# Performance work log

Measured on AMD Instinct MI355X. Metric: run time of the kernel, lower is better.

Reference implementation:

```python
import jax, jax.numpy as jnp
import numpy as np

N_API, N_FILE, E = 50000, 20000, 250000
N_INP, N_OUT, H = 512, 256, 3


def setup_inputs() -> dict:
    key = jax.random.key(0)
    ks = jax.random.split(key, 16)
    s = 0.05
    return {
        "emb_api": jax.random.normal(ks[0], (N_API, N_INP), jnp.float32),
        "emb_file": jax.random.normal(ks[1], (N_FILE, N_INP), jnp.float32),
        "e_tensor": jax.random.normal(ks[2], (E,), jnp.float32),
        "src": jax.random.randint(ks[3], (E,), 0, N_API, jnp.int32),
        "dst": jax.random.randint(ks[4], (E,), 0, N_FILE, jnp.int32),
        # api_proj / file_proj (Linear n_inp->n_inp), stored as [in,out]
        "Wapi": jax.random.normal(ks[5], (N_INP, N_INP), jnp.float32) * s,
        "bapi": jnp.zeros((N_INP,), jnp.float32),
        "Wfile": jax.random.normal(ks[6], (N_INP, N_INP), jnp.float32) * s,
        "bfile": jnp.zeros((N_INP,), jnp.float32),
        # GATConv fc_src / fc_dst (no bias), attn vectors, output bias
        "Wsrc": jax.random.normal(ks[7], (N_INP, H * N_OUT), jnp.float32) * s,
        "Wdst": jax.random.normal(ks[8], (N_INP, H * N_OUT), jnp.float32) * s,
        "attn_l": jax.random.normal(ks[9], (H, N_OUT), jnp.float32) * s,
        "attn_r": jax.random.normal(ks[10], (H, N_OUT), jnp.float32) * s,
        "gat_bias": jnp.zeros((H * N_OUT,), jnp.float32),
        # head_linear (3*n_out -> n_out)
        "Whead": jax.random.normal(ks[11], (H * N_OUT, N_OUT), jnp.float32) * s,
        "bhead": jnp.zeros((N_OUT,), jnp.float32),
    }


def reference(emb_api, emb_file, e_tensor, src, dst,
              Wapi, bapi, Wfile, bfile,
              Wsrc, Wdst, attn_l, attn_r, gat_bias,
              Whead, bhead):
    nd = emb_file.shape[0]
    # dual linear projections
    x_api = emb_api @ Wapi + bapi            # [Nsrc, n_inp]
    x_file = emb_file @ Wfile + bfile        # [Ndst, n_inp]
    # GATConv (bipartite, DGL semantics): per-head linear, additive attention
    fsrc = (x_api @ Wsrc).reshape(-1, H, N_OUT)   # [Nsrc, H, D]
    fdst = (x_file @ Wdst).reshape(-1, H, N_OUT)  # [Ndst, H, D]
    el = jnp.sum(fsrc * attn_l, axis=-1)          # [Nsrc, H]
    er = jnp.sum(fdst * attn_r, axis=-1)          # [Ndst, H]
    e = jax.nn.leaky_relu(el[src] + er[dst], 0.2)  # [E, H]
    # edge softmax over incoming edges of each dst node
    m = jax.ops.segment_max(e, dst, num_segments=nd)   # [Ndst, H]
    a = jnp.exp(e - m[dst])
    z = jax.ops.segment_sum(a, dst, num_segments=nd)   # [Ndst, H]
    alpha = a / z[dst]                                  # [E, H]
    # weighted aggregation of source messages
    rst = jax.ops.segment_sum(alpha[:, :, None] * fsrc[src], dst,
                              num_segments=nd)          # [Ndst, H, D]
    rst = rst + gat_bias.reshape(H, N_OUT)
    # head fusion
    z_str = rst.reshape(nd, H * N_OUT) @ Whead + bhead  # [Ndst, n_out]
    return z_str
```

## Files before the change

### kernel.cpp

```cpp
#include <hip/hip_runtime.h>
#include <hip/hip_bf16.h>
#include <cstdint>
#include <cstddef>

#define N_INP 512
#define N_OUT 256
#define H 3
#define HD (H * N_OUT)
#define AGG_D (H * (N_INP + 1))
#define HSTR 522
#define KP 1568
#define GEMM_NT (KP / 32)

typedef __attribute__((ext_vector_type(8))) short short8;
typedef __attribute__((ext_vector_type(4))) float f32x4;

__device__ inline unsigned short f2bf(float x) {
    union { float f; unsigned u; } v; v.f = x;
    unsigned r = v.u + 0x7fffu + ((v.u >> 16) & 1u);
    return (unsigned short)(r >> 16);
}
__device__ inline float bflo2f(unsigned u) {
    union { unsigned u; float f; } v; v.u = u << 16; return v.f;
}
__device__ inline float bfhi2f(unsigned u) {
    union { unsigned u; float f; } v; v.u = u & 0xffff0000u; return v.f;
}

__global__ void zero_int_kernel(int* p, int n) {
    int i = blockIdx.x * blockDim.x + threadIdx.x;
    if (i < n) p[i] = 0;
}

__global__ __launch_bounds__(256) void v_kernel(
    const float* __restrict__ Wsrc, const float* __restrict__ Wdst,
    const float* __restrict__ attn_l, const float* __restrict__ attn_r,
    float* __restrict__ v) {
    int wave = threadIdx.x >> 6, lane = threadIdx.x & 63;
    int idx = blockIdx.x * 4 + wave;
    if (idx >= 2 * H * N_INP) return;
    int which = idx / (H * N_INP);
    int r = idx % (H * N_INP);
    int h = r / N_INP, o = r % N_INP;
    const float* W = which ? Wdst : Wsrc;
    const float* at = which ? attn_r : attn_l;
    float s = 0.f;
#pragma unroll
    for (int i = 0; i < N_OUT / 64; ++i) {
        int t = lane + i * 64;
        s += W[(size_t)o * HD + h * N_OUT + t] * at[h * N_OUT + t];
    }
#pragma unroll
    for (int off = 32; off >= 1; off >>= 1) s += __shfl_xor(s, off, 64);
    if (lane == 0) v[idx] = s;
}

__global__ __launch_bounds__(256) void u_kernel(
    const float* __restrict__ Wapi, const float* __restrict__ Wfile,
    const float* __restrict__ bapi, const float* __restrict__ bfile,
    const float* __restrict__ v, float* __restrict__ u,
    float* __restrict__ ebias) {
    int wave = threadIdx.x >> 6, lane = threadIdx.x & 63;
    int idx = blockIdx.x * 4 + wave;
    if (idx < 2 * H * N_INP) {
        int which = idx / (H * N_INP);
        int r = idx % (H * N_INP);
        int h = r / N_INP, i = r % N_INP;
        const float* W = which ? Wfile : Wapi;
        const float* vv = v + which * (H * N_INP) + h * N_INP;
        float s = 0.f;
#pragma unroll
        for (int j = 0; j < N_INP / 64; ++j) {
            int o = lane + j * 64;
            s += W[(size_t)i * N_INP + o] * vv[o];
        }
#pragma unroll
        for (int off = 32; off >= 1; off >>= 1) s += __shfl_xor(s, off, 64);
        if (lane == 0) u[idx] = s;
    } else if (idx < 2 * H * N_INP + 6) {
        int k = idx - 2 * H * N_INP;
        int which = k / H, h = k % H;
        const float* b = which ? bfile : bapi;
        const float* vv = v + which * (H * N_INP) + h * N_INP;
        float s = 0.f;
#pragma unroll
        for (int j = 0; j < N_INP / 64; ++j) {
            int o = lane + j * 64;
            s += b[o] * vv[o];
        }
#pragma unroll
        for (int off = 32; off >= 1; off >>= 1) s += __shfl_xor(s, off, 64);
        if (lane == 0) ebias[k] = s;
    }
}

__global__ __launch_bounds__(256) void elr_kernel(
    const float* __restrict__ emb, const float* __restrict__ u,
    const float* __restrict__ ebias, float* __restrict__ out,
    unsigned short* __restrict__ embB, int n) {
    __shared__ float su[H * N_INP];
    for (int i = threadIdx.x; i < H * N_INP; i += 256) su[i] = u[i];
    __syncthreads();
    int wave = threadIdx.x >> 6;
    int lane = threadIdx.x & 63;
    int node = blockIdx.x * 4 + wave;
    if (node >= n) return;
    const float4* row = (const float4*)(emb + (size_t)node * N_INP);
    float4 v0 = row[lane];
    float4 v1 = row[64 + lane];
    int c0 = lane * 4, c1 = 256 + lane * 4;
    if (embB) {
        unsigned short* o = embB + (size_t)node * N_INP;
        ushort4 p0, p1;
        p0.x = f2bf(v0.x); p0.y = f2bf(v0.y); p0.z = f2bf(v0.z); p0.w = f2bf(v0.w);
        p1.x = f2bf(v1.x); p1.y = f2bf(v1.y); p1.z = f2bf(v1.z); p1.w = f2bf(v1.w);
        *(ushort4*)(o + c0) = p0;
        *(ushort4*)(o + c1) = p1;
    }
    float d[H];
#pragma unroll
    for (int h = 0; h < H; ++h) {
        const float* uh = su + h * N_INP;
        d[h] = v0.x * uh[c0] + v0.y * uh[c0 + 1] + v0.z * uh[c0 + 2] + v0.w * uh[c0 + 3]
             + v1.x * uh[c1] + v1.y * uh[c1 + 1] + v1.z * uh[c1 + 2] + v1.w * uh[c1 + 3];
#pragma unroll
        for (int off = 32; off >= 1; off >>= 1) d[h] += __shfl_xor(d[h], off, 64);
    }
    if (lane == 0) {
#pragma unroll
        for (int h = 0; h < H; ++h) out[(size_t)node * H + h] = d[h] + ebias[h];
    }
}

__global__ void count_kernel(const int* __restrict__ dst, int* __restrict__ counts, int E) {
    int e = blockIdx.x * blockDim.x + threadIdx.x;
    if (e < E) atomicAdd(&counts[dst[e]], 1);
}

__global__ __launch_bounds__(1024) void scan_kernel(const int* __restrict__ counts,
                                                    int* __restrict__ offsets,
                                                    int* __restrict__ cursor, int n) {
    __shared__ int part[1024];
    int t = threadIdx.x;
    const int CH = (n + 1023) / 1024;
    int lo = t * CH, hi = min(lo + CH, n);
    int s = 0;
    for (int i = lo; i < hi; ++i) s += counts[i];
    part[t] = s;
    __syncthreads();
    for (int off = 1; off < 1024; off <<= 1) {
        int v = (t >= off) ? part[t - off] : 0;
        __syncthreads();
        part[t] += v;
        __syncthreads();
    }
    int base = (t == 0) ? 0 : part[t - 1];
    for (int i = lo; i < hi; ++i) {
        offsets[i] = base; cursor[i] = base;
        base += counts[i];
    }
    if (t == 1023) offsets[n] = part[1023];
}

__global__ void scatter_kernel(const int* __restrict__ src, const int* __restrict__ dst,
                               int* __restrict__ cursor, int* __restrict__ csr_src, int E) {
    int e = blockIdx.x * blockDim.x + threadIdx.x;
    if (e < E) {
        int slot = atomicAdd(&cursor[dst[e]], 1);
        csr_src[slot] = src[e];
    }
}

__global__ __launch_bounds__(256) void alpha_kernel(
    const int* __restrict__ offsets, const int* __restrict__ csr_src,
    const float* __restrict__ el, const float* __restrict__ er,
    float* __restrict__ alpha, int nd) {
    int wave = threadIdx.x >> 6;
    int lane = threadIdx.x & 63;
    int d = blockIdx.x * 4 + wave;
    if (d >= nd) return;
    int lo = offsets[d], hi = offsets[d + 1];
    if (lo == hi) return;
    float er0 = er[(size_t)d * H + 0], er1 = er[(size_t)d * H + 1], er2 = er[(size_t)d * H + 2];
    float m0 = -3.4e38f, m1 = -3.4e38f, m2 = -3.4e38f;
    for (int s = lo + lane; s < hi; s += 64) {
        int u = csr_src[s];
        float e0 = el[(size_t)u * H + 0] + er0; e0 = e0 >= 0.f ? e0 : 0.2f * e0;
        float e1 = el[(size_t)u * H + 1] + er1; e1 = e1 >= 0.f ? e1 : 0.2f * e1;
        float e2 = el[(size_t)u * H + 2] + er2; e2 = e2 >= 0.f ? e2 : 0.2f * e2;
        m0 = fmaxf(m0, e0); m1 = fmaxf(m1, e1); m2 = fmaxf(m2, e2);
    }
#pragma unroll
    for (int off = 32; off >= 1; off >>= 1) {
        m0 = fmaxf(m0, __shfl_xor(m0, off, 64));
        m1 = fmaxf(m1, __shfl_xor(m1, off, 64));
        m2 = fmaxf(m2, __shfl_xor(m2, off, 64));
    }
    float s0 = 0.f, s1 = 0.f, s2 = 0.f;
    for (int s = lo + lane; s < hi; s += 64) {
        int u = csr_src[s];
        float e0 = el[(size_t)u * H + 0] + er0; e0 = e0 >= 0.f ? e0 : 0.2f * e0;
        float e1 = el[(size_t)u * H + 1] + er1; e1 = e1 >= 0.f ? e1 : 0.2f * e1;
        float e2 = el[(size_t)u * H + 2] + er2; e2 = e2 >= 0.f ? e2 : 0.2f * e2;
        float a0 = expf(e0 - m0), a1 = expf(e1 - m1), a2 = expf(e2 - m2);
        alpha[(size_t)s * H + 0] = a0; alpha[(size_t)s * H + 1] = a1; alpha[(size_t)s * H + 2] = a2;
        s0 += a0; s1 += a1; s2 += a2;
    }
#pragma unroll
    for (int off = 32; off >= 1; off >>= 1) {
        s0 += __shfl_xor(s0, off, 64);
        s1 += __shfl_xor(s1, off, 64);
        s2 += __shfl_xor(s2, off, 64);
    }
    float i0 = 1.f / s0, i1 = 1.f / s1, i2 = 1.f / s2;
    for (int s = lo + lane; s < hi; s += 64) {
        alpha[(size_t)s * H + 0] *= i0;
        alpha[(size_t)s * H + 1] *= i1;
        alpha[(size_t)s * H + 2] *= i2;
    }
}

#define AGG_CH 512
__global__ __launch_bounds__(256) void agg_kernel(
    const int* __restrict__ offsets, const int* __restrict__ csr_src,
    const float* __restrict__ alpha, const unsigned short* __restrict__ embB,
    unsigned short* __restrict__ aggB, int nd) {
    __shared__ int su[AGG_CH];
    __shared__ float sw0[AGG_CH], sw1[AGG_CH], sw2[AGG_CH];
    int d = blockIdx.x;
    if (d >= nd) return;
    int tid = threadIdx.x;
    int lo = offsets[d], hi = offsets[d + 1];
    const unsigned* ebdw = (const unsigned*)embB;
    float a00 = 0.f, a01 = 0.f, a10 = 0.f, a11 = 0.f, a20 = 0.f, a21 = 0.f;
    for (int base = lo; base < hi; base += AGG_CH) {
        int cnt = min(hi - base, AGG_CH);
        for (int i = tid; i < cnt; i += 256) {
            int s = base + i;
            su[i] = csr_src[s];
            sw0[i] = alpha[(size_t)s * H + 0];
            sw1[i] = alpha[(size_t)s * H + 1];
            sw2[i] = alpha[(size_t)s * H + 2];
        }
        __syncthreads();
        int i = 0;
        for (; i + 4 <= cnt; i += 4) {
            int u0 = su[i], u1 = su[i + 1], u2 = su[i + 2], u3 = su[i + 3];
            unsigned v0 = ebdw[((size_t)u0 << 8) + tid];
            unsigned v1 = ebdw[((size_t)u1 << 8) + tid];
            unsigned v2 = ebdw[((size_t)u2 << 8) + tid];
            unsigned v3 = ebdw[((size_t)u3 << 8) + tid];
            float w00 = sw0[i], w01 = sw1[i], w02 = sw2[i];
            float w10 = sw0[i+1], w11 = sw1[i+1], w12 = sw2[i+1];
            float w20 = sw0[i+2], w21 = sw1[i+2], w22 = sw2[i+2];
            float w30 = sw0[i+3], w31 = sw1[i+3], w32 = sw2[i+3];
            float x, y;
            x = bflo2f(v0); y = bfhi2f(v0);
            a00 += w00 * x; a01 += w00 * y; a10 += w01 * x; a11 += w01 * y; a20 += w02 * x; a21 += w02 * y;
            x = bflo2f(v1); y = bfhi2f(v1);
            a00 += w10 * x; a01 += w10 * y; a10 += w11 * x; a11 += w11 * y; a20 += w12 * x; a21 += w12 * y;
            x = bflo2f(v2); y = bfhi2f(v2);
            a00 += w20 * x; a01 += w20 * y; a10 += w21 * x; a11 += w21 * y; a20 += w22 * x; a21 += w22 * y;
            x = bflo2f(v3); y = bfhi2f(v3);
            a00 += w30 * x; a01 += w30 * y; a10 += w31 * x; a11 += w31 * y; a20 += w32 * x; a21 += w32 * y;
        }
        for (; i < cnt; ++i) {
            int u = su[i];
            unsigned v = ebdw[((size_t)u << 8) + tid];
            float w0 = sw0[i], w1 = sw1[i], w2 = sw2[i];
            float x = bflo2f(v), y = bfhi2f(v);
            a00 += w0 * x; a01 += w0 * y;
            a10 += w1 * x; a11 += w1 * y;
            a20 += w2 * x; a21 += w2 * y;
        }
        __syncthreads();
    }
    int c = tid * 2;
    size_t base = (size_t)d * KP;
    *(unsigned*)(aggB + base + 0 * HSTR + c) = (unsigned)f2bf(a00) | ((unsigned)f2bf(a01) << 16);
    *(unsigned*)(aggB + base + 1 * HSTR + c) = (unsigned)f2bf(a10) | ((unsigned)f2bf(a11) << 16);
    *(unsigned*)(aggB + base + 2 * HSTR + c) = (unsigned)f2bf(a20) | ((unsigned)f2bf(a21) << 16);
    if (tid == 0) {
        unsigned short flag = (hi > lo) ? (unsigned short)0x3f80 : (unsigned short)0;
#pragma unroll
        for (int h = 0; h < H; ++h) {
            aggB[base + h * HSTR + 512] = flag;
            for (int z = 513; z < HSTR; ++z) aggB[base + h * HSTR + z] = 0;
        }
        aggB[base + 3 * HSTR + 0] = 0;
        aggB[base + 3 * HSTR + 1] = 0;
    }
}

template <int K>
__global__ __launch_bounds__(256) void wgemm(
    const float* __restrict__ A, int lda, size_t sAz,
    const float* __restrict__ B, int ldb, size_t sBz,
    float* __restrict__ C, int ldc, size_t sCz, int M) {
    A += blockIdx.z * sAz; B += blockIdx.z * sBz; C += blockIdx.z * sCz;
    __shared__ float sA[8 * K];
    __shared__ float red[8 * 256];
    int tid = threadIdx.x;
    int r0 = blockIdx.x * 8;
    int bn = blockIdx.y * 64;
    for (int i = tid; i < 8 * K; i += 256) {
        int r = i / K, k = i % K;
        sA[i] = A[(size_t)(r0 + r) * lda + k];
    }
    __syncthreads();
    int cl = tid & 63, ks = tid >> 6;
    int col = bn + cl;
    const int KC = K / 4;
    float acc[8] = {};
    for (int k0 = ks * KC; k0 < ks * KC + KC; k0 += 8) {
        float b[8];
#pragma unroll
        for (int j = 0; j < 8; ++j) b[j] = B[(size_t)(k0 + j) * ldb + col];
#pragma unroll
        for (int j = 0; j < 8; ++j) {
            float bb = b[j];
#pragma unroll
            for (int i = 0; i < 8; ++i) acc[i] += sA[i * K + k0 + j] * bb;
        }
    }
#pragma unroll
    for (int i = 0; i < 8; ++i) red[i * 256 + ks * 64 + cl] = acc[i];
    __syncthreads();
    for (int t = tid; t < 512; t += 256) {
        int i = t >> 6, c = t & 63;
        float s = red[i * 256 + c] + red[i * 256 + 64 + c]
                + red[i * 256 + 128 + c] + red[i * 256 + 192 + c];
        if (r0 + i < M) C[(size_t)(r0 + i) * ldc + bn + c] = s;
    }
}

__global__ __launch_bounds__(256) void brow_kernel(
    const float* __restrict__ bapi, const float* __restrict__ T,
    const float* __restrict__ gat_bias, const float* __restrict__ Whead,
    const float* __restrict__ bhead,
    float* __restrict__ Mmat, float* __restrict__ bz) {
    int wave = threadIdx.x >> 6, lane = threadIdx.x & 63;
    int idx = blockIdx.x * 4 + wave;
    if (idx < H * N_OUT) {
        int h = idx / N_OUT, j = idx % N_OUT;
        float s = 0.f;
#pragma unroll
        for (int i = 0; i < N_INP / 64; ++i) {
            int cc = lane + i * 64;
            s += bapi[cc] * T[((size_t)h * N_INP + cc) * N_OUT + j];
        }
#pragma unroll
        for (int off = 32; off >= 1; off >>= 1) s += __shfl_xor(s, off, 64);
        if (lane == 0) Mmat[((size_t)(h * 513 + 512)) * N_OUT + j] = s;
    } else if (idx < H * N_OUT + N_OUT) {
        int j = idx - H * N_OUT;
        float s = 0.f;
#pragma unroll
        for (int i = 0; i < HD / 64; ++i) {
            int f = lane + i * 64;
            s += gat_bias[f] * Whead[(size_t)f * N_OUT + j];
        }
#pragma unroll
        for (int off = 32; off >= 1; off >>= 1) s += __shfl_xor(s, off, 64);
        if (lane == 0) bz[j] = s + bhead[j];
    }
}

__global__ void convT_kernel(const float* __restrict__ Mmat, unsigned short* __restrict__ MmatT) {
    int idx = blockIdx.x * blockDim.x + threadIdx.x;
    if (idx >= N_OUT * KP) return;
    int n = idx / KP, k = idx % KP;
    float v = 0.f;
    if (k < H * HSTR) {
        int h = k / HSTR, c = k % HSTR;
        if (c < 513) v = Mmat[((size_t)(h * 513 + c)) * N_OUT + n];
    }
    MmatT[(size_t)n * KP + k] = f2bf(v);
}

__global__ __launch_bounds__(256) void gemm_mfma(
    const unsigned short* __restrict__ A, const unsigned short* __restrict__ BT,
    const float* __restrict__ bias, float* __restrict__ C, int M) {
    __shared__ __align__(16) short As[2][32 * 32];
    __shared__ __align__(16) short Bs[2][256 * 32];
    int tid = threadIdx.x;
    int wave = tid >> 6, lane = tid & 63;
    int bm = blockIdx.x * 32;
    int wn = wave * 64;
    int quad = lane >> 4, m16 = lane & 15;

    int srow = tid >> 2;
    int schunk = (tid & 3) * 8;
    bool doA = (tid < 128);
    int arow_l = doA ? srow : 0;
    int arow = bm + arow_l; if (arow >= M) arow = M - 1;
    const unsigned short* Ap  = A + (size_t)arow * KP + schunk;
    const unsigned short* Bp0 = BT + (size_t)(srow      ) * KP + schunk;
    const unsigned short* Bp1 = BT + (size_t)(srow +  64) * KP + schunk;
    const unsigned short* Bp2 = BT + (size_t)(srow + 128) * KP + schunk;
    const unsigned short* Bp3 = BT + (size_t)(srow + 192) * KP + schunk;

    f32x4 acc[2][4] = {};
    short8 a0{}, b00{}, b01{}, b02{}, b03{};
    short8 a1{}, b10{}, b11{}, b12{}, b13{};

    auto LD = [&](short8& ra, short8& r0, short8& r1, short8& r2, short8& r3, int k0) {
        if (doA) ra = *(const short8*)(Ap + k0);
        r0 = *(const short8*)(Bp0 + k0);
        r1 = *(const short8*)(Bp1 + k0);
        r2 = *(const short8*)(Bp2 + k0);
        r3 = *(const short8*)(Bp3 + k0);
    };
    auto WR = [&](int buf, short8 ra, short8 r0, short8 r1, short8 r2, short8 r3) {
        if (doA) *(short8*)(&As[buf][arow_l * 32 + schunk]) = ra;
        *(short8*)(&Bs[buf][(srow      ) * 32 + schunk]) = r0;
        *(short8*)(&Bs[buf][(srow +  64) * 32 + schunk]) = r1;
        *(short8*)(&Bs[buf][(srow + 128) * 32 + schunk]) = r2;
        *(short8*)(&Bs[buf][(srow + 192) * 32 + schunk]) = r3;
    };
    auto FENCE = [&]() {
        asm volatile("s_waitcnt lgkmcnt(0)" ::: "memory");
        __builtin_amdgcn_sched_barrier(0);
        __builtin_amdgcn_s_barrier();
        __builtin_amdgcn_sched_barrier(0);
    };

    LD(a0, b00, b01, b02, b03, 0);
    LD(a1, b10, b11, b12, b13, 32);
    WR(0, a0, b00, b01, b02, b03);
    LD(a0, b00, b01, b02, b03, 64);
    FENCE();

    for (int t = 0; t < GEMM_NT; ++t) {
        int rb = t & 1;
        short8 af[2], bf[4];
#pragma unroll
        for (int mt = 0; mt < 2; ++mt)
            af[mt] = *(const short8*)(&As[rb][(mt * 16 + m16) * 32 + quad * 8]);
#pragma unroll
        for (int nt = 0; nt < 4; ++nt)
            bf[nt] = *(const short8*)(&Bs[rb][(wn + nt * 16 + m16) * 32 + quad * 8]);
        int k3 = (t + 3) * 32;
        if (t & 1) {
            if (t + 1 < GEMM_NT) WR(rb ^ 1, a0, b00, b01, b02, b03);
            if (t + 3 < GEMM_NT) LD(a0, b00, b01, b02, b03, k3);
        } else {
            if (t + 1 < GEMM_NT) WR(rb ^ 1, a1, b10, b11, b12, b13);
            if (t + 3 < GEMM_NT) LD(a1, b10, b11, b12, b13, k3);
        }
#pragma unroll
        for (int mt = 0; mt < 2; ++mt)
#pragma unroll
            for (int nt = 0; nt < 4; ++nt)
                acc[mt][nt] = __builtin_amdgcn_mfma_f32_16x16x32_bf16(
                    af[mt], bf[nt], acc[mt][nt], 0, 0, 0);
        FENCE();
    }

    float bcol[4];
#pragma unroll
    for (int nt = 0; nt < 4; ++nt) bcol[nt] = bias[wn + nt * 16 + m16];
#pragma unroll
    for (int mt = 0; mt < 2; ++mt) {
#pragma unroll
        for (int i = 0; i < 4; ++i) {
            int r = bm + mt * 16 + quad * 4 + i;
            if (r >= M) continue;
#pragma unroll
            for (int nt = 0; nt < 4; ++nt) {
                int col = wn + nt * 16 + m16;
                C[(size_t)r * N_OUT + col] = acc[mt][nt][i] + bcol[nt];
            }
        }
    }
}

extern "C" void kernel_launch(void* const* d_in, const int* in_sizes, int n_in,
                              void* d_out, int out_size, void* d_ws, size_t ws_size,
                              hipStream_t stream) {
    const float* emb_api  = (const float*)d_in[0];
    const float* emb_file = (const float*)d_in[1];
    const int*   src      = (const int*)d_in[3];
    const int*   dst      = (const int*)d_in[4];
    const float* Wapi     = (const float*)d_in[5];
    const float* bapi     = (const float*)d_in[6];
    const float* Wfile    = (const float*)d_in[7];
    const float* bfile    = (const float*)d_in[8];
    const float* Wsrc     = (const float*)d_in[9];
    const float* Wdst     = (const float*)d_in[10];
    const float* attn_l   = (const float*)d_in[11];
    const float* attn_r   = (const float*)d_in[12];
    const float* gat_bias = (const float*)d_in[13];
    const float* Whead    = (const float*)d_in[14];
    const float* bhead    = (const float*)d_in[15];
    float* out = (float*)d_out;

    const int NAPI = in_sizes[0] / N_INP;
    const int NFIL = in_sizes[1] / N_INP;
    const int E    = in_sizes[3];

    char* p = (char*)d_ws;
    auto alloc = [&](size_t bytes) -> void* {
        void* r = (void*)p;
        p += (bytes + 255) & ~(size_t)255;
        return r;
    };
    float* el      = (float*)alloc((size_t)NAPI * H * 4);
    float* er      = (float*)alloc((size_t)NFIL * H * 4);
    float* vbuf    = (float*)alloc(2 * H * N_INP * 4);
    float* ubuf    = (float*)alloc(2 * H * N_INP * 4);
    float* ebias   = (float*)alloc(8 * 4);
    float* T       = (float*)alloc((size_t)H * N_INP * N_OUT * 4);
    float* Mmat    = (float*)alloc((size_t)AGG_D * N_OUT * 4);
    float* bz      = (float*)alloc(N_OUT * 4);
    int*   counts  = (int*)alloc((size_t)NFIL * 4);
    int*   offsets = (int*)alloc((size_t)(NFIL + 1) * 4);
    int*   cursor  = (int*)alloc((size_t)NFIL * 4);
    int*   csr_src = (int*)alloc((size_t)E * 4);
    float* alphaB  = (float*)alloc((size_t)E * H * 4);
    unsigned short* embB  = (unsigned short*)alloc((size_t)NAPI * N_INP * 2);
    unsigned short* aggB  = (unsigned short*)alloc((size_t)NFIL * KP * 2);
    unsigned short* MmatT = (unsigned short*)alloc((size_t)N_OUT * KP * 2);
    (void)ws_size; (void)n_in; (void)out_size;

    v_kernel<<<(2 * H * N_INP + 3) / 4, 256, 0, stream>>>(Wsrc, Wdst, attn_l, attn_r, vbuf);
    u_kernel<<<(2 * H * N_INP + 6 + 3) / 4, 256, 0, stream>>>(Wapi, Wfile, bapi, bfile, vbuf, ubuf, ebias);
    wgemm<N_OUT><<<dim3(N_INP / 8, 4, H), 256, 0, stream>>>(
        Wsrc, HD, (size_t)N_OUT,
        Whead, N_OUT, (size_t)N_OUT * N_OUT,
        T, N_OUT, (size_t)N_INP * N_OUT, N_INP);
    wgemm<N_INP><<<dim3(N_INP / 8, 4, H), 256, 0, stream>>>(
        Wapi, N_INP, (size_t)0,
        T, N_OUT, (size_t)N_INP * N_OUT,
        Mmat, N_OUT, (size_t)513 * N_OUT, N_INP);
    brow_kernel<<<(H * N_OUT + N_OUT + 3) / 4, 256, 0, stream>>>(
        bapi, T, gat_bias, Whead, bhead, Mmat, bz);
    convT_kernel<<<(N_OUT * KP + 255) / 256, 256, 0, stream>>>(Mmat, MmatT);

    elr_kernel<<<(NAPI + 3) / 4, 256, 0, stream>>>(emb_api, ubuf, ebias, el, embB, NAPI);
    elr_kernel<<<(NFIL + 3) / 4, 256, 0, stream>>>(emb_file, ubuf + H * N_INP, ebias + 3, er, nullptr, NFIL);

    zero_int_kernel<<<(NFIL + 255) / 256, 256, 0, stream>>>(counts, NFIL);
    count_kernel<<<(E + 255) / 256, 256, 0, stream>>>(dst, counts, E);
    scan_kernel<<<1, 1024, 0, stream>>>(counts, offsets, cursor, NFIL);
    scatter_kernel<<<(E + 255) / 256, 256, 0, stream>>>(src, dst, cursor, csr_src, E);

    alpha_kernel<<<(NFIL + 3) / 4, 256, 0, stream>>>(offsets, csr_src, el, er, alphaB, NFIL);
    agg_kernel<<<NFIL, 256, 0, stream>>>(offsets, csr_src, alphaB, embB, aggB, NFIL);

    gemm_mfma<<<dim3((NFIL + 31) / 32), 256, 0, stream>>>(
        aggB, MmatT, bz, out, NFIL);
}
```

Before: 436.0 us.

## Enlarge GEMM block tile to 64 rows with 8 waves and pad LDS rows

The final MFMA GEMM now uses 512-thread blocks covering 64 output rows instead of 32, so each staged B tile is shared by twice as many rows and global loads of the weight matrix per output row are halved. LDS rows are padded from 32 to 40 shorts to reduce bank conflicts on the fragment reads. In exchange the grid has half as many blocks (about 313), which may lower occupancy on a many-CU device, and LDS use per block grows.

Measured after the change: 438.0 us. Within noise of the previous version (+0.5%).

```diff
diff --git a/kernel.cpp b/kernel.cpp
--- a/kernel.cpp
+++ b/kernel.cpp
@@ -11,6 +11,7 @@
 #define HSTR 522
 #define KP 1568
 #define GEMM_NT (KP / 32)
+#define LSTR 40
 
 typedef __attribute__((ext_vector_type(8))) short short8;
 typedef __attribute__((ext_vector_type(4))) float f32x4;
@@ -378,45 +379,40 @@
     MmatT[(size_t)n * KP + k] = f2bf(v);
 }
 
-__global__ __launch_bounds__(256) void gemm_mfma(
+__global__ __launch_bounds__(512) void gemm_mfma(
     const unsigned short* __restrict__ A, const unsigned short* __restrict__ BT,
     const float* __restrict__ bias, float* __restrict__ C, int M) {
-    __shared__ __align__(16) short As[2][32 * 32];
-    __shared__ __align__(16) short Bs[2][256 * 32];
+    __shared__ __align__(16) short As[2][64 * LSTR];
+    __shared__ __align__(16) short Bs[2][256 * LSTR];
     int tid = threadIdx.x;
     int wave = tid >> 6, lane = tid & 63;
-    int bm = blockIdx.x * 32;
-    int wn = wave * 64;
+    int bm = blockIdx.x * 64;
+    int wm = (wave >> 2) * 32;
+    int wn = (wave & 3) * 64;
     int quad = lane >> 4, m16 = lane & 15;
 
     int srow = tid >> 2;
     int schunk = (tid & 3) * 8;
-    bool doA = (tid < 128);
+    bool doA = (tid < 256);
     int arow_l = doA ? srow : 0;
     int arow = bm + arow_l; if (arow >= M) arow = M - 1;
     const unsigned short* Ap  = A + (size_t)arow * KP + schunk;
     const unsigned short* Bp0 = BT + (size_t)(srow      ) * KP + schunk;
-    const unsigned short* Bp1 = BT + (size_t)(srow +  64) * KP + schunk;
-    const unsigned short* Bp2 = BT + (size_t)(srow + 128) * KP + schunk;
-    const unsigned short* Bp3 = BT + (size_t)(srow + 192) * KP + schunk;
+    const unsigned short* Bp1 = BT + (size_t)(srow + 128) * KP + schunk;
 
     f32x4 acc[2][4] = {};
-    short8 a0{}, b00{}, b01{}, b02{}, b03{};
-    short8 a1{}, b10{}, b11{}, b12{}, b13{};
-
-    auto LD = [&](short8& ra, short8& r0, short8& r1, short8& r2, short8& r3, int k0) {
+    short8 a0{}, b00{}, b01{};
+    short8 a1{}, b10{}, b11{};
+
+    auto LD = [&](short8& ra, short8& r0, short8& r1, int k0) {
         if (doA) ra = *(const short8*)(Ap + k0);
         r0 = *(const short8*)(Bp0 + k0);
         r1 = *(const short8*)(Bp1 + k0);
-        r2 = *(const short8*)(Bp2 + k0);
-        r3 = *(const short8*)(Bp3 + k0);
     };
-    auto WR = [&](int buf, short8 ra, short8 r0, short8 r1, short8 r2, short8 r3) {
-        if (doA) *(short8*)(&As[buf][arow_l * 32 + schunk]) = ra;
-        *(short8*)(&Bs[buf][(srow      ) * 32 + schunk]) = r0;
-        *(short8*)(&Bs[buf][(srow +  64) * 32 + schunk]) = r1;
-        *(short8*)(&Bs[buf][(srow + 128) * 32 + schunk]) = r2;
-        *(short8*)(&Bs[buf][(srow + 192) * 32 + schunk]) = r3;
+    auto WR = [&](int buf, short8 ra, short8 r0, short8 r1) {
+        if (doA) *(short8*)(&As[buf][arow_l * LSTR + schunk]) = ra;
+        *(short8*)(&Bs[buf][(srow      ) * LSTR + schunk]) = r0;
+        *(short8*)(&Bs[buf][(srow + 128) * LSTR + schunk]) = r1;
     };
     auto FENCE = [&]() {
         asm volatile("s_waitcnt lgkmcnt(0)" ::: "memory");
@@ -425,10 +421,10 @@
         __builtin_amdgcn_sched_barrier(0);
     };
 
-    LD(a0, b00, b01, b02, b03, 0);
-    LD(a1, b10, b11, b12, b13, 32);
-    WR(0, a0, b00, b01, b02, b03);
-    LD(a0, b00, b01, b02, b03, 64);
+    LD(a0, b00, b01, 0);
+    LD(a1, b10, b11, 32);
+    WR(0, a0, b00, b01);
+    LD(a0, b00, b01, 64);
     FENCE();
 
     for (int t = 0; t < GEMM_NT; ++t) {
@@ -436,17 +432,17 @@
         short8 af[2], bf[4];
 #pragma unroll
         for (int mt = 0; mt < 2; ++mt)
-            af[mt] = *(const short8*)(&As[rb][(mt * 16 + m16) * 32 + quad * 8]);
+            af[mt] = *(const short8*)(&As[rb][(wm + mt * 16 + m16) * LSTR + quad * 8]);
 #pragma unroll
         for (int nt = 0; nt < 4; ++nt)
-            bf[nt] = *(const short8*)(&Bs[rb][(wn + nt * 16 + m16) * 32 + quad * 8]);
+            bf[nt] = *(const short8*)(&Bs[rb][(wn + nt * 16 + m16) * LSTR + quad * 8]);
         int k3 = (t + 3) * 32;
         if (t & 1) {
-            if (t + 1 < GEMM_NT) WR(rb ^ 1, a0, b00, b01, b02, b03);
-            if (t + 3 < GEMM_NT) LD(a0, b00, b01, b02, b03, k3);
+            if (t + 1 < GEMM_NT) WR(rb ^ 1, a0, b00, b01);
+            if (t + 3 < GEMM_NT) LD(a0, b00, b01, k3);
         } else {
-            if (t + 1 < GEMM_NT) WR(rb ^ 1, a1, b10, b11, b12, b13);
-            if (t + 3 < GEMM_NT) LD(a1, b10, b11, b12, b13, k3);
+            if (t + 1 < GEMM_NT) WR(rb ^ 1, a1, b10, b11);
+            if (t + 3 < GEMM_NT) LD(a1, b10, b11, k3);
         }
 #pragma unroll
         for (int mt = 0; mt < 2; ++mt)
@@ -464,7 +460,7 @@
     for (int mt = 0; mt < 2; ++mt) {
 #pragma unroll
         for (int i = 0; i < 4; ++i) {
-            int r = bm + mt * 16 + quad * 4 + i;
+            int r = bm + wm + mt * 16 + quad * 4 + i;
             if (r >= M) continue;
 #pragma unroll
             for (int nt = 0; nt < 4; ++nt) {
@@ -548,6 +544,6 @@
     alpha_kernel<<<(NFIL + 3) / 4, 256, 0, stream>>>(offsets, csr_src, el, er, alphaB, NFIL);
     agg_kernel<<<NFIL, 256, 0, stream>>>(offsets, csr_src, alphaB, embB, aggB, NFIL);
 
-    gemm_mfma<<<dim3((NFIL + 31) / 32), 256, 0, stream>>>(
+    gemm_mfma<<<dim3((NFIL + 63) / 64), 512, 0, stream>>>(
         aggB, MmatT, bz, out, NFIL);
 }
```
